# Kernel optimization log

Hardware: AMD Instinct MI355X
Metric: run time of the kernel (lower is better)

Reference implementation:

```python
import jax, jax.numpy as jnp
import numpy as np

N = 10000
E = 320000
D = 256
EPS = 1e-5

def layer_norm(x, g, b):
    mu = jnp.mean(x, axis=-1, keepdims=True)
    var = jnp.mean(jnp.square(x - mu), axis=-1, keepdims=True)
    return (x - mu) * jax.lax.rsqrt(var + EPS) * g + b

def linear(x, w, b):
    # w: [in, out]
    return x @ w + b

def setup_inputs() -> dict:
    key = jax.random.key(0)
    ks = jax.random.split(key, 20)
    s = 1.0 / np.sqrt(D)
    inp = {
        'x': jax.random.normal(ks[0], (N, D), jnp.float32),
        'edge_index': jax.random.randint(ks[1], (2, E), 0, N, jnp.int64),
        'edge_weight': jax.random.normal(ks[2], (E,), jnp.float32),
        'wq': jax.random.normal(ks[3], (D, D), jnp.float32) * s,
        'bq': jnp.zeros((D,), jnp.float32),
        'wk': jax.random.normal(ks[4], (D, D), jnp.float32) * s,
        'bk': jnp.zeros((D,), jnp.float32),
        'wv': jax.random.normal(ks[5], (D, D), jnp.float32) * s,
        'bv': jnp.zeros((D,), jnp.float32),
        'ws': jax.random.normal(ks[6], (D, D), jnp.float32) * s,
        'bs': jnp.zeros((D,), jnp.float32),
        'we': jax.random.normal(ks[7], (1, 1), jnp.float32),
        'be': jnp.zeros((1,), jnp.float32),
        'g1': jnp.ones((D,), jnp.float32),
        'b1': jnp.zeros((D,), jnp.float32),
        'g2': jnp.ones((D,), jnp.float32),
        'b2': jnp.zeros((D,), jnp.float32),
        'w_ff1': jax.random.normal(ks[8], (D, 2 * D), jnp.float32) * s,
        'b_ff1': jnp.zeros((2 * D,), jnp.float32),
        'w_ff2': jax.random.normal(ks[9], (2 * D, D), jnp.float32) * (1.0 / np.sqrt(2 * D)),
        'b_ff2': jnp.zeros((D,), jnp.float32),
    }
    return inp

def reference(x, edge_index, edge_weight, wq, bq, wk, bk, wv, bv, ws, bs, we, be,
              g1, b1, g2, b2, w_ff1, b_ff1, w_ff2, b_ff2):
    n = x.shape[0]
    scale = x.shape[-1] ** (-0.5)
    q = linear(x, wq, bq)
    k = linear(x, wk, bk)
    v = linear(x, wv, bv)
    src, dst = edge_index[0], edge_index[1]
    # per-edge attention scores: dot(q[dst], k[src]) * scale
    scores = jnp.sum(q[dst] * k[src], axis=-1) * scale
    scores = scores + (edge_weight[:, None] @ we + be)[:, 0]
    # two-pass segment softmax over dst
    seg_max = jax.ops.segment_max(scores, dst, num_segments=n)
    exp_s = jnp.exp(scores - seg_max[dst])
    denom = jax.ops.segment_sum(exp_s, dst, num_segments=n)
    attn = exp_s / jnp.maximum(denom[dst], 1e-12)
    # scatter-add weighted messages
    message = v[src] * attn[:, None]  # [E, D]
    out = jax.ops.segment_sum(message, dst, num_segments=n)
    x = layer_norm(x + out + linear(x, ws, bs), g1, b1)
    ffn = linear(jax.nn.gelu(linear(x, w_ff1, b_ff1)), w_ff2, b_ff2)
    x = layer_norm(x + ffn, g2, b2)
    return x
```

## Files before the change

kernel.cpp:

```cpp
#include <hip/hip_runtime.h>
#include <math.h>

#define N_NODES 10000
#define N_EDGES 320000
#define DIM 256
#define BCAP 128

#define P_PARTS 250
#define NPP 40
#define PCAP 2048
#define EPT 16

typedef __attribute__((ext_vector_type(8))) short bf16x8;
typedef __attribute__((ext_vector_type(4))) float fx4;

typedef __attribute__((address_space(3))) unsigned lds_u32;
typedef __attribute__((address_space(1))) const unsigned gbl_u32;


__device__ __forceinline__ float gelu_tanh(float x) {
  const float k0 = 0.7978845608028654f;
  float x3 = x * x * x;
  return 0.5f * x * (1.0f + tanhf(k0 * (x + 0.044715f * x3)));
}

__device__ __forceinline__ unsigned short f2bf(float f) {
  unsigned u = __float_as_uint(f);
  unsigned r = 0x7FFFu + ((u >> 16) & 1u);
  return (unsigned short)((u + r) >> 16);
}

__device__ __forceinline__ float bf_lo(unsigned u) { return __uint_as_float(u << 16); }
__device__ __forceinline__ float bf_hi(unsigned u) { return __uint_as_float(u & 0xFFFF0000u); }


#define SEG_QKVS 262144
#define SEG_FF1 131072
#define SEG_FF2 131072
#define SEG_BIAS 1024
#define SEG_CONV 320000
#define SEG_ZCNT 256
#define PREP_TOTAL (SEG_QKVS + SEG_FF1 + SEG_FF2 + SEG_BIAS + SEG_CONV + SEG_ZCNT)

__global__ __launch_bounds__(256) void prep_all_kernel(
    const float* __restrict__ wq, const float* __restrict__ wk,
    const float* __restrict__ wv, const float* __restrict__ ws,
    const float* __restrict__ bq, const float* __restrict__ bk,
    const float* __restrict__ bv, const float* __restrict__ bs,
    const float* __restrict__ wff1, const float* __restrict__ wff2,
    const float* __restrict__ x,
    unsigned short* __restrict__ wt_qkvs, float* __restrict__ bias_qkvs,
    unsigned short* __restrict__ wt_ff1, unsigned short* __restrict__ wt_ff2,
    unsigned short* __restrict__ xb, unsigned* __restrict__ pcnt) {
  int id = blockIdx.x * 256 + threadIdx.x;
  if (id < SEG_QKVS) {
    const int n = id >> 8, k = id & 255;
    const float* w = (n < 256) ? wq : (n < 512) ? wk : (n < 768) ? wv : ws;
    wt_qkvs[id] = f2bf(w[k * 256 + (n & 255)]);
    return;
  }
  id -= SEG_QKVS;
  if (id < SEG_FF1) {
    const int n = id >> 8, k = id & 255;
    wt_ff1[id] = f2bf(wff1[k * 512 + n]);
    return;
  }
  id -= SEG_FF1;
  if (id < SEG_FF2) {
    const int n = id >> 9, k = id & 511;
    wt_ff2[id] = f2bf(wff2[k * 256 + n]);
    return;
  }
  id -= SEG_FF2;
  if (id < SEG_BIAS) {
    bias_qkvs[id] = (id < 256) ? bq[id] : (id < 512) ? bk[id & 255]
                    : (id < 768) ? bv[id & 255] : bs[id & 255];
    return;
  }
  id -= SEG_BIAS;
  if (id < SEG_CONV) {
    const int base = id * 8;
    float4 a = *(const float4*)(x + base);
    float4 b = *(const float4*)(x + base + 4);
    unsigned short h[8] = {f2bf(a.x), f2bf(a.y), f2bf(a.z), f2bf(a.w),
                           f2bf(b.x), f2bf(b.y), f2bf(b.z), f2bf(b.w)};
    *(uint4*)(xb + base) = *(const uint4*)h;
    return;
  }
  id -= SEG_CONV;
  if (id < SEG_ZCNT) pcnt[id] = 0u;
}

__global__ __launch_bounds__(512) void scatter_p1(
    const int* __restrict__ ei, const float* __restrict__ ew,
    const float* __restrict__ we, const float* __restrict__ be,
    unsigned* __restrict__ pcnt, uint2* __restrict__ pbuf) {
  __shared__ unsigned lcnt[P_PARTS];
  __shared__ unsigned lbase[P_PARTS];
  const int tid = threadIdx.x;
  for (int i = tid; i < P_PARTS; i += 512) lcnt[i] = 0;
  __syncthreads();
  const float wes = we[0], bes = be[0];
  const int e0 = blockIdx.x * (512 * EPT);

  unsigned pp[EPT];
  unsigned rr[EPT];
  unsigned sv[EPT];
  float ebv[EPT];
#pragma unroll
  for (int j = 0; j < EPT; j++) {
    const int e = e0 + j * 512 + tid;
    pp[j] = 0;
    rr[j] = 0xFFFFFFFFu;
    if (e < N_EDGES) {
      const int dst = ei[N_EDGES + e];
      const int src = ei[e];
      const int p = dst / NPP;
      sv[j] = (unsigned)dst | ((unsigned)src << 16);
      ebv[j] = fmaf(ew[e], wes, bes);
      pp[j] = (unsigned)p;
      rr[j] = atomicAdd(&lcnt[p], 1u);
    }
  }
  __syncthreads();
  for (int i = tid; i < P_PARTS; i += 512) {
    const unsigned c = lcnt[i];
    lbase[i] = c ? atomicAdd(&pcnt[i], c) : 0u;
  }
  __syncthreads();
#pragma unroll
  for (int j = 0; j < EPT; j++) {
    if (rr[j] != 0xFFFFFFFFu) {
      const unsigned pos = lbase[pp[j]] + rr[j];
      if (pos < PCAP) {
        uint2 rec;
        rec.x = sv[j];
        rec.y = __float_as_uint(ebv[j]);
        pbuf[(size_t)pp[j] * PCAP + pos] = rec;
      }
    }
  }
}

__global__ __launch_bounds__(256) void scatter_p2(
    const unsigned* __restrict__ pcnt, const uint2* __restrict__ pbuf,
    unsigned* __restrict__ cnt, uint2* __restrict__ es_csr) {
  __shared__ unsigned lcnt[NPP];
  const int p = blockIdx.x;
  const int tid = threadIdx.x;
  if (tid < NPP) lcnt[tid] = 0;
  __syncthreads();
  const int n0 = p * NPP;
  const int tot = min((int)pcnt[p], PCAP);
  for (int i = tid; i < tot; i += 256) {
    const uint2 rec = pbuf[(size_t)p * PCAP + i];
    const int dst = (int)(rec.x & 0xFFFFu);
    const int src = (int)(rec.x >> 16);
    const unsigned r = atomicAdd(&lcnt[dst - n0], 1u);
    if (r < BCAP) {
      uint2 o;
      o.x = (unsigned)src;
      o.y = rec.y;
      es_csr[(size_t)dst * BCAP + r] = o;
    }
  }
  __syncthreads();
  if (tid < NPP) cnt[n0 + tid] = lcnt[tid];
}

template <int GELU, int WF32, int WB16, int SPLIT>
__global__ __launch_bounds__(256) void mfma_gemm(
    const unsigned short* __restrict__ A, int lda,
    const unsigned short* __restrict__ Bt,
    const float* __restrict__ bias,
    const float* __restrict__ xres,
    float* __restrict__ C, int ldc,
    unsigned short* __restrict__ Cb, int ldcb,
    int M, int K) {
  __shared__ char lds[32768];
  const int tid = threadIdx.x;

  const int l = tid & 63;
  const int wid = tid >> 6;
  const int wrow = (wid & 1) * 32;
  const int wcol = (wid >> 1) * 32;
  const int bm = blockIdx.y * 64;
  const int bn = blockIdx.x * 64;

  fx4 acc[2][2];
#pragma unroll
  for (int i = 0; i < 2; i++)
#pragma unroll
    for (int j = 0; j < 2; j++) acc[i][j] = (fx4)(0.0f);

#define STAGE(BUFOFF, KB)                                                      \
  {                                                                            \
    _Pragma("unroll") for (int i = 0; i < 2; i++) {                            \
      const int id = i * 256 + tid;                                            \
      const int row = id >> 3;                                                 \
      const int ccs = (id & 7) ^ (row & 7);                                    \
      __builtin_amdgcn_global_load_lds(                                        \
          (gbl_u32*)(A + (size_t)(bm + row) * lda + (KB) + ccs * 8),           \
          (lds_u32*)(lds + (BUFOFF) + id * 16), 16, 0, 0);                     \
    }                                                                          \
    _Pragma("unroll") for (int i = 0; i < 2; i++) {                            \
      const int id = i * 256 + tid;                                            \
      const int row = id >> 3;                                                 \
      const int ccs = (id & 7) ^ (row & 7);                                    \
      __builtin_amdgcn_global_load_lds(                                        \
          (gbl_u32*)(Bt + (size_t)(bn + row) * K + (KB) + ccs * 8),            \
          (lds_u32*)(lds + (BUFOFF) + 8192 + id * 16), 16, 0, 0);              \
    }                                                                          \
  }

  STAGE(0, 0);

  unsigned cur = 0;
  for (int kb = 0; kb < K; kb += 64) {
    if (kb + 64 < K) {
      STAGE((cur ^ 1) * 16384, kb + 64);
      asm volatile("s_waitcnt vmcnt(4)" ::: "memory");
    } else {
      asm volatile("s_waitcnt vmcnt(0)" ::: "memory");
    }
    __builtin_amdgcn_s_barrier();
    __builtin_amdgcn_sched_barrier(0);

    const char* As = lds + cur * 16384;
    const char* Bs = As + 8192;
#pragma unroll
    for (int kk = 0; kk < 2; kk++) {
      const int kbyte = (kk * 64 + ((l >> 4) << 4)) ^ ((l & 7) << 4);
      bf16x8 af[2], bg[2];
#pragma unroll
      for (int f = 0; f < 2; f++) {
        const int ar = wrow + f * 16 + (l & 15);
        af[f] = *(const bf16x8*)(As + ar * 128 + kbyte);
        const int br = wcol + f * 16 + (l & 15);
        bg[f] = *(const bf16x8*)(Bs + br * 128 + kbyte);
      }
#pragma unroll
      for (int fr = 0; fr < 2; fr++)
#pragma unroll
        for (int fc = 0; fc < 2; fc++)
          acc[fr][fc] = __builtin_amdgcn_mfma_f32_16x16x32_bf16(
              bg[fc], af[fr], acc[fr][fc], 0, 0, 0);
    }
    __builtin_amdgcn_s_barrier();
    cur ^= 1;
  }
#undef STAGE

#pragma unroll
  for (int fr = 0; fr < 2; fr++) {
    const int m = bm + wrow + fr * 16 + (l & 15);
    if (m < M) {
#pragma unroll
      for (int fc = 0; fc < 2; fc++) {
        const int n0 = bn + wcol + fc * 16 + ((l >> 4) << 2);
        const float4 b4 = *(const float4*)(bias + n0);
        fx4 v = acc[fr][fc];
        float o0 = v[0] + b4.x;
        float o1 = v[1] + b4.y;
        float o2 = v[2] + b4.z;
        float o3 = v[3] + b4.w;
        if (GELU) {
          o0 = gelu_tanh(o0); o1 = gelu_tanh(o1);
          o2 = gelu_tanh(o2); o3 = gelu_tanh(o3);
        }
        if (SPLIT) {
          const int seg = n0 >> 8, nn = n0 & 255;
          if (seg == 3) {
            const float4 xr = *(const float4*)(xres + (size_t)m * 256 + nn);
            float4 w;
            w.x = o0 + xr.x; w.y = o1 + xr.y; w.z = o2 + xr.z; w.w = o3 + xr.w;
            *(float4*)(C + (size_t)m * 256 + nn) = w;
          } else {
            uint2 pk;
            pk.x = (unsigned)f2bf(o0) | ((unsigned)f2bf(o1) << 16);
            pk.y = (unsigned)f2bf(o2) | ((unsigned)f2bf(o3) << 16);
            *(uint2*)(Cb + (size_t)seg * (N_NODES * DIM) + (size_t)m * 256 + nn) = pk;
          }
        } else {
          if (WF32) {
            float4 w; w.x = o0; w.y = o1; w.z = o2; w.w = o3;
            *(float4*)(C + (size_t)m * ldc + n0) = w;
          }
          if (WB16) {
            uint2 pk;
            pk.x = (unsigned)f2bf(o0) | ((unsigned)f2bf(o1) << 16);
            pk.y = (unsigned)f2bf(o2) | ((unsigned)f2bf(o3) << 16);
            *(uint2*)(Cb + (size_t)m * ldcb + n0) = pk;
          }
        }
      }
    }
  }
}

__global__ __launch_bounds__(64) void agg_fused_kernel(
    const unsigned* __restrict__ cnt, const uint2* __restrict__ es_csr,
    const unsigned short* __restrict__ qb,
    const unsigned short* __restrict__ kb, const unsigned short* __restrict__ vb,
    const float* __restrict__ sbuf,
    const float* __restrict__ g, const float* __restrict__ b,
    float* __restrict__ out, unsigned short* __restrict__ outb) {
  const int node = blockIdx.x;
  const int lane = threadIdx.x;
  const int grp = lane >> 4;
  const int t = lane & 15;
  const int start = node * BCAP;
  const int deg = min((int)cnt[node], BCAP);
  const int end = start + deg;

  const uint4 qA = *(const uint4*)(qb + (size_t)node * 256 + t * 16);
  const uint4 qB = *(const uint4*)(qb + (size_t)node * 256 + t * 16 + 8);
  float qf[16];
  qf[0] = bf_lo(qA.x);  qf[1] = bf_hi(qA.x);
  qf[2] = bf_lo(qA.y);  qf[3] = bf_hi(qA.y);
  qf[4] = bf_lo(qA.z);  qf[5] = bf_hi(qA.z);
  qf[6] = bf_lo(qA.w);  qf[7] = bf_hi(qA.w);
  qf[8] = bf_lo(qB.x);  qf[9] = bf_hi(qB.x);
  qf[10] = bf_lo(qB.y); qf[11] = bf_hi(qB.y);
  qf[12] = bf_lo(qB.z); qf[13] = bf_hi(qB.z);
  qf[14] = bf_lo(qB.w); qf[15] = bf_hi(qB.w);

  float m = -3.4e38f, dsum = 0.f;
  float a0 = 0.f, a1 = 0.f, a2 = 0.f, a3 = 0.f;

  int ea = start + grp * 2;
  int eb_ = ea + 1;
  bool va = ea < end, vbd = eb_ < end;
  int sa = 0, sb = 0;
  float ba = 0.f, bb = 0.f;
  if (va) { const uint2 es = es_csr[ea]; sa = (int)es.x; ba = __uint_as_float(es.y); }
  if (vbd) { const uint2 es = es_csr[eb_]; sb = (int)es.x; bb = __uint_as_float(es.y); }
  uint4 kAa = *(const uint4*)(kb + (size_t)sa * 256 + t * 16);
  uint4 kBa = *(const uint4*)(kb + (size_t)sa * 256 + t * 16 + 8);
  uint4 kAb = *(const uint4*)(kb + (size_t)sb * 256 + t * 16);
  uint4 kBb = *(const uint4*)(kb + (size_t)sb * 256 + t * 16 + 8);

  for (int base = start; base < end; base += 8) {
    const int s0 = __shfl(sa, 0), s1 = __shfl(sa, 16);
    const int s2 = __shfl(sa, 32), s3 = __shfl(sa, 48);
    const int s4 = __shfl(sb, 0), s5 = __shfl(sb, 16);
    const int s6 = __shfl(sb, 32), s7 = __shfl(sb, 48);
    const uint2 v0 = *(const uint2*)(vb + (size_t)s0 * 256 + lane * 4);
    const uint2 v1 = *(const uint2*)(vb + (size_t)s1 * 256 + lane * 4);
    const uint2 v2 = *(const uint2*)(vb + (size_t)s2 * 256 + lane * 4);
    const uint2 v3 = *(const uint2*)(vb + (size_t)s3 * 256 + lane * 4);
    const uint2 v4 = *(const uint2*)(vb + (size_t)s4 * 256 + lane * 4);
    const uint2 v5 = *(const uint2*)(vb + (size_t)s5 * 256 + lane * 4);
    const uint2 v6 = *(const uint2*)(vb + (size_t)s6 * 256 + lane * 4);
    const uint2 v7 = *(const uint2*)(vb + (size_t)s7 * 256 + lane * 4);

    const int na = base + 8 + grp * 2;
    const int nb = na + 1;
    const bool va_n = na < end, vb_n = nb < end;
    int sa_n = 0, sb_n = 0;
    float ba_n = 0.f, bb_n = 0.f;
    if (va_n) { const uint2 es = es_csr[na]; sa_n = (int)es.x; ba_n = __uint_as_float(es.y); }
    if (vb_n) { const uint2 es = es_csr[nb]; sb_n = (int)es.x; bb_n = __uint_as_float(es.y); }

    float da = qf[0] * bf_lo(kAa.x);
    float db = qf[0] * bf_lo(kAb.x);
    da = fmaf(qf[1], bf_hi(kAa.x), da);  db = fmaf(qf[1], bf_hi(kAb.x), db);
    da = fmaf(qf[2], bf_lo(kAa.y), da);  db = fmaf(qf[2], bf_lo(kAb.y), db);
    da = fmaf(qf[3], bf_hi(kAa.y), da);  db = fmaf(qf[3], bf_hi(kAb.y), db);
    da = fmaf(qf[4], bf_lo(kAa.z), da);  db = fmaf(qf[4], bf_lo(kAb.z), db);
    da = fmaf(qf[5], bf_hi(kAa.z), da);  db = fmaf(qf[5], bf_hi(kAb.z), db);
    da = fmaf(qf[6], bf_lo(kAa.w), da);  db = fmaf(qf[6], bf_lo(kAb.w), db);
    da = fmaf(qf[7], bf_hi(kAa.w), da);  db = fmaf(qf[7], bf_hi(kAb.w), db);
    da = fmaf(qf[8], bf_lo(kBa.x), da);  db = fmaf(qf[8], bf_lo(kBb.x), db);
    da = fmaf(qf[9], bf_hi(kBa.x), da);  db = fmaf(qf[9], bf_hi(kBb.x), db);
    da = fmaf(qf[10], bf_lo(kBa.y), da); db = fmaf(qf[10], bf_lo(kBb.y), db);
    da = fmaf(qf[11], bf_hi(kBa.y), da); db = fmaf(qf[11], bf_hi(kBb.y), db);
    da = fmaf(qf[12], bf_lo(kBa.z), da); db = fmaf(qf[12], bf_lo(kBb.z), db);
    da = fmaf(qf[13], bf_hi(kBa.z), da); db = fmaf(qf[13], bf_hi(kBb.z), db);
    da = fmaf(qf[14], bf_lo(kBa.w), da); db = fmaf(qf[14], bf_lo(kBb.w), db);
    da = fmaf(qf[15], bf_hi(kBa.w), da); db = fmaf(qf[15], bf_hi(kBb.w), db);
    da += __shfl_xor(da, 1);  db += __shfl_xor(db, 1);
    da += __shfl_xor(da, 2);  db += __shfl_xor(db, 2);
    da += __shfl_xor(da, 4);  db += __shfl_xor(db, 4);
    da += __shfl_xor(da, 8);  db += __shfl_xor(db, 8);
    const float sca = va ? fmaf(da, 0.0625f, ba) : -3.4e38f;
    const float scb = vbd ? fmaf(db, 0.0625f, bb) : -3.4e38f;

    const uint4 kAa_n = *(const uint4*)(kb + (size_t)sa_n * 256 + t * 16);
    const uint4 kBa_n = *(const uint4*)(kb + (size_t)sa_n * 256 + t * 16 + 8);
    const uint4 kAb_n = *(const uint4*)(kb + (size_t)sb_n * 256 + t * 16);
    const uint4 kBb_n = *(const uint4*)(kb + (size_t)sb_n * 256 + t * 16 + 8);

    const float c0 = __shfl(sca, 0), c1 = __shfl(sca, 16);
    const float c2 = __shfl(sca, 32), c3 = __shfl(sca, 48);
    const float c4 = __shfl(scb, 0), c5 = __shfl(scb, 16);
    const float c6 = __shfl(scb, 32), c7 = __shfl(scb, 48);

    const float mx = fmaxf(fmaxf(fmaxf(c0, c1), fmaxf(c2, c3)),
                           fmaxf(fmaxf(c4, c5), fmaxf(c6, c7)));
    const float mn = fmaxf(m, mx);
    const float scale = __expf(m - mn);
    const float w0 = __expf(c0 - mn), w1 = __expf(c1 - mn);
    const float w2 = __expf(c2 - mn), w3 = __expf(c3 - mn);
    const float w4 = __expf(c4 - mn), w5 = __expf(c5 - mn);
    const float w6 = __expf(c6 - mn), w7 = __expf(c7 - mn);
    dsum = fmaf(dsum, scale, ((w0 + w1) + (w2 + w3)) + ((w4 + w5) + (w6 + w7)));

    float t0 = a0 * scale;
    t0 = fmaf(w0, bf_lo(v0.x), t0); t0 = fmaf(w1, bf_lo(v1.x), t0);
    t0 = fmaf(w2, bf_lo(v2.x), t0); t0 = fmaf(w3, bf_lo(v3.x), t0);
    t0 = fmaf(w4, bf_lo(v4.x), t0); t0 = fmaf(w5, bf_lo(v5.x), t0);
    t0 = fmaf(w6, bf_lo(v6.x), t0); t0 = fmaf(w7, bf_lo(v7.x), t0);
    a0 = t0;
    float t1 = a1 * scale;
    t1 = fmaf(w0, bf_hi(v0.x), t1); t1 = fmaf(w1, bf_hi(v1.x), t1);
    t1 = fmaf(w2, bf_hi(v2.x), t1); t1 = fmaf(w3, bf_hi(v3.x), t1);
    t1 = fmaf(w4, bf_hi(v4.x), t1); t1 = fmaf(w5, bf_hi(v5.x), t1);
    t1 = fmaf(w6, bf_hi(v6.x), t1); t1 = fmaf(w7, bf_hi(v7.x), t1);
    a1 = t1;
    float t2 = a2 * scale;
    t2 = fmaf(w0, bf_lo(v0.y), t2); t2 = fmaf(w1, bf_lo(v1.y), t2);
    t2 = fmaf(w2, bf_lo(v2.y), t2); t2 = fmaf(w3, bf_lo(v3.y), t2);
    t2 = fmaf(w4, bf_lo(v4.y), t2); t2 = fmaf(w5, bf_lo(v5.y), t2);
    t2 = fmaf(w6, bf_lo(v6.y), t2); t2 = fmaf(w7, bf_lo(v7.y), t2);
    a2 = t2;
    float t3 = a3 * scale;
    t3 = fmaf(w0, bf_hi(v0.y), t3); t3 = fmaf(w1, bf_hi(v1.y), t3);
    t3 = fmaf(w2, bf_hi(v2.y), t3); t3 = fmaf(w3, bf_hi(v3.y), t3);
    t3 = fmaf(w4, bf_hi(v4.y), t3); t3 = fmaf(w5, bf_hi(v5.y), t3);
    t3 = fmaf(w6, bf_hi(v6.y), t3); t3 = fmaf(w7, bf_hi(v7.y), t3);
    a3 = t3;
    m = mn;

    sa = sa_n; sb = sb_n;
    ba = ba_n; bb = bb_n;
    va = va_n; vbd = vb_n;
    kAa = kAa_n; kBa = kBa_n;
    kAb = kAb_n; kBb = kBb_n;
  }
  const float inv = 1.0f / fmaxf(dsum, 1e-12f);

  const float4 sv = *(const float4*)(sbuf + (size_t)node * 256 + lane * 4);
  float r0 = a0 * inv + sv.x;
  float r1 = a1 * inv + sv.y;
  float r2 = a2 * inv + sv.z;
  float r3 = a3 * inv + sv.w;

  float sum = r0 + r1 + r2 + r3;
#pragma unroll
  for (int off = 32; off > 0; off >>= 1) sum += __shfl_xor(sum, off);
  const float mu = sum * (1.0f / 256.0f);
  const float d0 = r0 - mu, d1 = r1 - mu, d2 = r2 - mu, d3 = r3 - mu;
  float vs = d0 * d0 + d1 * d1 + d2 * d2 + d3 * d3;
#pragma unroll
  for (int off = 32; off > 0; off >>= 1) vs += __shfl_xor(vs, off);
  const float rs = rsqrtf(vs * (1.0f / 256.0f) + 1e-5f);

  const float4 gv = *(const float4*)(g + lane * 4);
  const float4 bv = *(const float4*)(b + lane * 4);
  float4 o;
  o.x = d0 * rs * gv.x + bv.x;
  o.y = d1 * rs * gv.y + bv.y;
  o.z = d2 * rs * gv.z + bv.z;
  o.w = d3 * rs * gv.w + bv.w;
  *(float4*)(out + (size_t)node * 256 + lane * 4) = o;
  uint2 pk;
  pk.x = (unsigned)f2bf(o.x) | ((unsigned)f2bf(o.y) << 16);
  pk.y = (unsigned)f2bf(o.z) | ((unsigned)f2bf(o.w) << 16);
  *(uint2*)(outb + (size_t)node * 256 + lane * 4) = pk;
}


__global__ __launch_bounds__(256) void ln2_kernel(
    const float* __restrict__ x1, const float* __restrict__ y,
    const float* __restrict__ g, const float* __restrict__ b,
    float* __restrict__ out) {
  __shared__ float red[4];
  const int row = blockIdx.x;
  const int t = threadIdx.x;
  float v = x1[(size_t)row * 256 + t] + y[(size_t)row * 256 + t];
  float s = v;
#pragma unroll
  for (int off = 32; off > 0; off >>= 1) s += __shfl_xor(s, off);
  if ((t & 63) == 0) red[t >> 6] = s;
  __syncthreads();
  float tot = red[0] + red[1] + red[2] + red[3];
  __syncthreads();
  const float mu = tot * (1.0f / 256.0f);
  const float d = v - mu;
  float vs = d * d;
#pragma unroll
  for (int off = 32; off > 0; off >>= 1) vs += __shfl_xor(vs, off);
  if ((t & 63) == 0) red[t >> 6] = vs;
  __syncthreads();
  float vtot = red[0] + red[1] + red[2] + red[3];
  const float r = rsqrtf(vtot * (1.0f / 256.0f) + 1e-5f);
  out[(size_t)row * 256 + t] = d * r * g[t] + b[t];
}


extern "C" void kernel_launch(void* const* d_in, const int* in_sizes, int n_in,
                              void* d_out, int out_size, void* d_ws,
                              size_t ws_size, hipStream_t stream) {
  const float* x = (const float*)d_in[0];
  const int* ei = (const int*)d_in[1];
  const float* ew = (const float*)d_in[2];
  const float* wq = (const float*)d_in[3];
  const float* bq = (const float*)d_in[4];
  const float* wk = (const float*)d_in[5];
  const float* bk = (const float*)d_in[6];
  const float* wv = (const float*)d_in[7];
  const float* bv = (const float*)d_in[8];
  const float* wsm = (const float*)d_in[9];
  const float* bs = (const float*)d_in[10];
  const float* we = (const float*)d_in[11];
  const float* be = (const float*)d_in[12];
  const float* g1 = (const float*)d_in[13];
  const float* b1 = (const float*)d_in[14];
  const float* g2 = (const float*)d_in[15];
  const float* b2 = (const float*)d_in[16];
  const float* wff1 = (const float*)d_in[17];
  const float* bff1 = (const float*)d_in[18];
  const float* wff2 = (const float*)d_in[19];
  const float* bff2 = (const float*)d_in[20];
  float* out = (float*)d_out;

  unsigned short* qb = (unsigned short*)d_ws;
  unsigned short* kbp = qb + 2560000;
  unsigned short* vbp = qb + 5120000;
  float* sbuf = (float*)(qb + 7680000);
  uint2* es_csr = (uint2*)(sbuf + 2560000);
  unsigned* cnt = (unsigned*)(es_csr + (size_t)N_NODES * BCAP);
  float* x1 = (float*)(cnt + N_NODES);
  float* y = x1 + 2560000;
  unsigned short* x1b = (unsigned short*)(y + 2560000);
  unsigned short* h_b = x1b + 2560000;
  unsigned short* xb = h_b;
  unsigned short* wt_qkvs = h_b + 5120000;
  unsigned short* wt_ff1 = wt_qkvs + 262144;
  unsigned short* wt_ff2 = wt_ff1 + 131072;
  float* bias_qkvs = (float*)(wt_ff2 + 131072);
  unsigned* pcnt = (unsigned*)(bias_qkvs + 1024);
  uint2* pbuf = (uint2*)(pcnt + 256);

  dim3 blk(256);
  const int mb = (N_NODES + 63) / 64;

  prep_all_kernel<<<(PREP_TOTAL + 255) / 256, blk, 0, stream>>>(
      wq, wk, wv, wsm, bq, bk, bv, bs, wff1, wff2, x,
      wt_qkvs, bias_qkvs, wt_ff1, wt_ff2, xb, pcnt);

  scatter_p1<<<(N_EDGES + 512 * EPT - 1) / (512 * EPT), dim3(512), 0, stream>>>(
      ei, ew, we, be, pcnt, pbuf);
  scatter_p2<<<P_PARTS, blk, 0, stream>>>(pcnt, pbuf, cnt, es_csr);

  mfma_gemm<0, 0, 0, 1><<<dim3(16, mb), blk, 0, stream>>>(
      xb, 256, wt_qkvs, bias_qkvs, x, sbuf, 0, qb, 0, N_NODES, 256);

  agg_fused_kernel<<<N_NODES, dim3(64), 0, stream>>>(
      cnt, es_csr, qb, kbp, vbp, sbuf, g1, b1, x1, x1b);

  mfma_gemm<1, 0, 1, 0><<<dim3(8, mb), blk, 0, stream>>>(
      x1b, 256, wt_ff1, bff1, nullptr, (float*)nullptr, 0, h_b, 512, N_NODES, 256);

  mfma_gemm<0, 1, 0, 0><<<dim3(4, mb), blk, 0, stream>>>(
      h_b, 512, wt_ff2, bff2, nullptr, y, 256, (unsigned short*)nullptr, 0, N_NODES, 512);

  ln2_kernel<<<N_NODES, blk, 0, stream>>>(x1, y, g2, b2, out);
}
```

Measured before the change: 125.6 us.

## Replace double-buffered LDS GEMM with register-resident A and full-K B tile in LDS

Rewrites the MFMA GEMM so each wave keeps its 16-row A slice for the whole K range in registers, loaded straight from global memory. The block's whole B (weight) tile is staged into swizzled LDS once, with a single barrier. This removes the per-K-step staging loop and its barriers. In exchange it uses more registers, larger LDS (up to 32KB), smaller per-wave M tiles, and no overlap between loads and compute. FF2 now uses 32-column tiles, doubling the grid width.

```diff
diff --git a/kernel.cpp b/kernel.cpp
--- a/kernel.cpp
+++ b/kernel.cpp
@@ -13,9 +13,6 @@
 
 typedef __attribute__((ext_vector_type(8))) short bf16x8;
 typedef __attribute__((ext_vector_type(4))) float fx4;
-
-typedef __attribute__((address_space(3))) unsigned lds_u32;
-typedef __attribute__((address_space(1))) const unsigned gbl_u32;
 
 
 __device__ __forceinline__ float gelu_tanh(float x) {
@@ -168,131 +165,100 @@
   if (tid < NPP) cnt[n0 + tid] = lcnt[tid];
 }
 
-template <int GELU, int WF32, int WB16, int SPLIT>
-__global__ __launch_bounds__(256) void mfma_gemm(
-    const unsigned short* __restrict__ A, int lda,
+template <int K, int NT, int GELU, int WF32, int WB16, int SPLIT>
+__global__ __launch_bounds__(256) void stream_gemm(
+    const unsigned short* __restrict__ A,
     const unsigned short* __restrict__ Bt,
     const float* __restrict__ bias,
     const float* __restrict__ xres,
     float* __restrict__ C, int ldc,
     unsigned short* __restrict__ Cb, int ldcb,
-    int M, int K) {
-  __shared__ char lds[32768];
+    int M) {
+  __shared__ char lds[NT * K * 2];
   const int tid = threadIdx.x;
-
   const int l = tid & 63;
-  const int wid = tid >> 6;
-  const int wrow = (wid & 1) * 32;
-  const int wcol = (wid >> 1) * 32;
+  const int w = tid >> 6;
+  const int bn = blockIdx.x * NT;
   const int bm = blockIdx.y * 64;
-  const int bn = blockIdx.x * 64;
-
-  fx4 acc[2][2];
-#pragma unroll
-  for (int i = 0; i < 2; i++)
-#pragma unroll
-    for (int j = 0; j < 2; j++) acc[i][j] = (fx4)(0.0f);
-
-#define STAGE(BUFOFF, KB)                                                      \
-  {                                                                            \
-    _Pragma("unroll") for (int i = 0; i < 2; i++) {                            \
-      const int id = i * 256 + tid;                                            \
-      const int row = id >> 3;                                                 \
-      const int ccs = (id & 7) ^ (row & 7);                                    \
-      __builtin_amdgcn_global_load_lds(                                        \
-          (gbl_u32*)(A + (size_t)(bm + row) * lda + (KB) + ccs * 8),           \
-          (lds_u32*)(lds + (BUFOFF) + id * 16), 16, 0, 0);                     \
-    }                                                                          \
-    _Pragma("unroll") for (int i = 0; i < 2; i++) {                            \
-      const int id = i * 256 + tid;                                            \
-      const int row = id >> 3;                                                 \
-      const int ccs = (id & 7) ^ (row & 7);                                    \
-      __builtin_amdgcn_global_load_lds(                                        \
-          (gbl_u32*)(Bt + (size_t)(bn + row) * K + (KB) + ccs * 8),            \
-          (lds_u32*)(lds + (BUFOFF) + 8192 + id * 16), 16, 0, 0);              \
-    }                                                                          \
-  }
-
-  STAGE(0, 0);
-
-  unsigned cur = 0;
-  for (int kb = 0; kb < K; kb += 64) {
-    if (kb + 64 < K) {
-      STAGE((cur ^ 1) * 16384, kb + 64);
-      asm volatile("s_waitcnt vmcnt(4)" ::: "memory");
+  const int wr = bm + w * 16;
+
+  constexpr int KS = K / 32;
+  constexpr int NF = NT / 16;
+  constexpr int CPR = K / 8;
+  constexpr int CPT = (NT * CPR) / 256;
+
+  uint4 af[KS];
+  {
+    const unsigned short* arow = A + (size_t)(wr + (l & 15)) * K + ((l >> 4) * 8);
+#pragma unroll
+    for (int kk = 0; kk < KS; kk++)
+      af[kk] = *(const uint4*)(arow + kk * 32);
+  }
+
+#pragma unroll
+  for (int i = 0; i < CPT; i++) {
+    const int ch = i * 256 + tid;
+    const int n = ch / CPR;
+    const int c = ch % CPR;
+    const uint4 v = *(const uint4*)(Bt + (size_t)(bn + n) * K + c * 8);
+    *(uint4*)(lds + n * (K * 2) + ((c * 16) ^ ((n & 7) << 4))) = v;
+  }
+  __syncthreads();
+
+  fx4 acc[NF];
+#pragma unroll
+  for (int nf = 0; nf < NF; nf++) acc[nf] = (fx4)(0.0f);
+#pragma unroll
+  for (int kk = 0; kk < KS; kk++) {
+    const bf16x8 a = *(const bf16x8*)(&af[kk]);
+#pragma unroll
+    for (int nf = 0; nf < NF; nf++) {
+      const int n = nf * 16 + (l & 15);
+      const bf16x8 b = *(const bf16x8*)(
+          lds + n * (K * 2) + ((kk * 64 + ((l >> 4) << 4)) ^ ((n & 7) << 4)));
+      acc[nf] = __builtin_amdgcn_mfma_f32_16x16x32_bf16(b, a, acc[nf], 0, 0, 0);
+    }
+  }
+
+  const int m = wr + (l & 15);
+  if (m >= M) return;
+  const int seg = bn >> 8;
+#pragma unroll
+  for (int nf = 0; nf < NF; nf++) {
+    const int n0 = bn + nf * 16 + ((l >> 4) << 2);
+    const float4 b4 = *(const float4*)(bias + n0);
+    fx4 v = acc[nf];
+    float o0 = v[0] + b4.x;
+    float o1 = v[1] + b4.y;
+    float o2 = v[2] + b4.z;
+    float o3 = v[3] + b4.w;
+    if (GELU) {
+      o0 = gelu_tanh(o0); o1 = gelu_tanh(o1);
+      o2 = gelu_tanh(o2); o3 = gelu_tanh(o3);
+    }
+    if (SPLIT) {
+      const int nn = n0 & 255;
+      if (seg == 3) {
+        const float4 xr = *(const float4*)(xres + (size_t)m * 256 + nn);
+        float4 wv;
+        wv.x = o0 + xr.x; wv.y = o1 + xr.y; wv.z = o2 + xr.z; wv.w = o3 + xr.w;
+        *(float4*)(C + (size_t)m * 256 + nn) = wv;
+      } else {
+        uint2 pk;
+        pk.x = (unsigned)f2bf(o0) | ((unsigned)f2bf(o1) << 16);
+        pk.y = (unsigned)f2bf(o2) | ((unsigned)f2bf(o3) << 16);
+        *(uint2*)(Cb + (size_t)seg * (N_NODES * DIM) + (size_t)m * 256 + nn) = pk;
+      }
     } else {
-      asm volatile("s_waitcnt vmcnt(0)" ::: "memory");
-    }
-    __builtin_amdgcn_s_barrier();
-    __builtin_amdgcn_sched_barrier(0);
-
-    const char* As = lds + cur * 16384;
-    const char* Bs = As + 8192;
-#pragma unroll
-    for (int kk = 0; kk < 2; kk++) {
-      const int kbyte = (kk * 64 + ((l >> 4) << 4)) ^ ((l & 7) << 4);
-      bf16x8 af[2], bg[2];
-#pragma unroll
-      for (int f = 0; f < 2; f++) {
-        const int ar = wrow + f * 16 + (l & 15);
-        af[f] = *(const bf16x8*)(As + ar * 128 + kbyte);
-        const int br = wcol + f * 16 + (l & 15);
-        bg[f] = *(const bf16x8*)(Bs + br * 128 + kbyte);
+      if (WF32) {
+        float4 wv; wv.x = o0; wv.y = o1; wv.z = o2; wv.w = o3;
+        *(float4*)(C + (size_t)m * ldc + n0) = wv;
       }
-#pragma unroll
-      for (int fr = 0; fr < 2; fr++)
-#pragma unroll
-        for (int fc = 0; fc < 2; fc++)
-          acc[fr][fc] = __builtin_amdgcn_mfma_f32_16x16x32_bf16(
-              bg[fc], af[fr], acc[fr][fc], 0, 0, 0);
-    }
-    __builtin_amdgcn_s_barrier();
-    cur ^= 1;
-  }
-#undef STAGE
-
-#pragma unroll
-  for (int fr = 0; fr < 2; fr++) {
-    const int m = bm + wrow + fr * 16 + (l & 15);
-    if (m < M) {
-#pragma unroll
-      for (int fc = 0; fc < 2; fc++) {
-        const int n0 = bn + wcol + fc * 16 + ((l >> 4) << 2);
-        const float4 b4 = *(const float4*)(bias + n0);
-        fx4 v = acc[fr][fc];
-        float o0 = v[0] + b4.x;
-        float o1 = v[1] + b4.y;
-        float o2 = v[2] + b4.z;
-        float o3 = v[3] + b4.w;
-        if (GELU) {
-          o0 = gelu_tanh(o0); o1 = gelu_tanh(o1);
-          o2 = gelu_tanh(o2); o3 = gelu_tanh(o3);
-        }
-        if (SPLIT) {
-          const int seg = n0 >> 8, nn = n0 & 255;
-          if (seg == 3) {
-            const float4 xr = *(const float4*)(xres + (size_t)m * 256 + nn);
-            float4 w;
-            w.x = o0 + xr.x; w.y = o1 + xr.y; w.z = o2 + xr.z; w.w = o3 + xr.w;
-            *(float4*)(C + (size_t)m * 256 + nn) = w;
-          } else {
-            uint2 pk;
-            pk.x = (unsigned)f2bf(o0) | ((unsigned)f2bf(o1) << 16);
-            pk.y = (unsigned)f2bf(o2) | ((unsigned)f2bf(o3) << 16);
-            *(uint2*)(Cb + (size_t)seg * (N_NODES * DIM) + (size_t)m * 256 + nn) = pk;
-          }
-        } else {
-          if (WF32) {
-            float4 w; w.x = o0; w.y = o1; w.z = o2; w.w = o3;
-            *(float4*)(C + (size_t)m * ldc + n0) = w;
-          }
-          if (WB16) {
-            uint2 pk;
-            pk.x = (unsigned)f2bf(o0) | ((unsigned)f2bf(o1) << 16);
-            pk.y = (unsigned)f2bf(o2) | ((unsigned)f2bf(o3) << 16);
-            *(uint2*)(Cb + (size_t)m * ldcb + n0) = pk;
-          }
-        }
+      if (WB16) {
+        uint2 pk;
+        pk.x = (unsigned)f2bf(o0) | ((unsigned)f2bf(o1) << 16);
+        pk.y = (unsigned)f2bf(o2) | ((unsigned)f2bf(o3) << 16);
+        *(uint2*)(Cb + (size_t)m * ldcb + n0) = pk;
       }
     }
   }
@@ -478,7 +444,8 @@
   __shared__ float red[4];
   const int row = blockIdx.x;
   const int t = threadIdx.x;
-  float v = x1[(size_t)row * 256 + t] + y[(size_t)row * 256 + t];
+  const size_t idx = (size_t)row * 256 + t;
+  float v = x1[idx] + y[idx];
   float s = v;
 #pragma unroll
   for (int off = 32; off > 0; off >>= 1) s += __shfl_xor(s, off);
@@ -495,7 +462,7 @@
   __syncthreads();
   float vtot = red[0] + red[1] + red[2] + red[3];
   const float r = rsqrtf(vtot * (1.0f / 256.0f) + 1e-5f);
-  out[(size_t)row * 256 + t] = d * r * g[t] + b[t];
+  out[idx] = d * r * g[t] + b[t];
 }
 
 
@@ -554,17 +521,17 @@
       ei, ew, we, be, pcnt, pbuf);
   scatter_p2<<<P_PARTS, blk, 0, stream>>>(pcnt, pbuf, cnt, es_csr);
 
-  mfma_gemm<0, 0, 0, 1><<<dim3(16, mb), blk, 0, stream>>>(
-      xb, 256, wt_qkvs, bias_qkvs, x, sbuf, 0, qb, 0, N_NODES, 256);
+  stream_gemm<256, 64, 0, 0, 0, 1><<<dim3(16, mb), blk, 0, stream>>>(
+      xb, wt_qkvs, bias_qkvs, x, sbuf, 0, qb, 0, N_NODES);
 
   agg_fused_kernel<<<N_NODES, dim3(64), 0, stream>>>(
       cnt, es_csr, qb, kbp, vbp, sbuf, g1, b1, x1, x1b);
 
-  mfma_gemm<1, 0, 1, 0><<<dim3(8, mb), blk, 0, stream>>>(
-      x1b, 256, wt_ff1, bff1, nullptr, (float*)nullptr, 0, h_b, 512, N_NODES, 256);
-
-  mfma_gemm<0, 1, 0, 0><<<dim3(4, mb), blk, 0, stream>>>(
-      h_b, 512, wt_ff2, bff2, nullptr, y, 256, (unsigned short*)nullptr, 0, N_NODES, 512);
+  stream_gemm<256, 64, 1, 0, 1, 0><<<dim3(8, mb), blk, 0, stream>>>(
+      x1b, wt_ff1, bff1, nullptr, (float*)nullptr, 0, h_b, 512, N_NODES);
+
+  stream_gemm<512, 32, 0, 1, 0, 0><<<dim3(8, mb), blk, 0, stream>>>(
+      h_b, wt_ff2, bff2, nullptr, y, 256, (unsigned short*)nullptr, 0, N_NODES);
 
   ln2_kernel<<<N_NODES, blk, 0, stream>>>(x1, y, g2, b2, out);
 }
```

Result: slower. 140.5 us (+11.9%).

## Fuse both FFN GEMMs into one kernel keeping hidden activations in LDS

Applied to the files above, without the earlier changes.

Replaces the two FFN GEMM launches with a single kernel. Each 256-thread block computes a 16-row tile of the GELU hidden layer with MFMA, stores it as bf16 in swizzled shared memory, and then immediately runs the second GEMM from LDS. This removes the global write and reread of the 10000x512 hidden tensor and one launch. In exchange, weights are read directly from global memory with no LDS staging, and small 16-row tiles mean weight traffic is repeated across 625 blocks. Also includes a minor index cleanup in the final layer-norm kernel.

```diff
diff --git a/kernel.cpp b/kernel.cpp
--- a/kernel.cpp
+++ b/kernel.cpp
@@ -298,6 +298,83 @@
   }
 }
 
+__global__ __launch_bounds__(256) void ffn_fused(
+    const unsigned short* __restrict__ x1b,
+    const unsigned short* __restrict__ w1,
+    const float* __restrict__ b1,
+    const unsigned short* __restrict__ w2,
+    const float* __restrict__ b2,
+    float* __restrict__ y, int M) {
+  __shared__ char hlds[16 * 1024];
+  const int tid = threadIdx.x;
+  const int l = tid & 63;
+  const int wv = tid >> 6;
+  const int bm = blockIdx.x * 16;
+  const int ml = l & 15;
+  const int kc = l >> 4;
+  const int swz = (ml & 7) << 4;
+
+  uint4 af[8];
+  {
+    const unsigned short* ar = x1b + (size_t)(bm + ml) * 256 + kc * 8;
+#pragma unroll
+    for (int kk = 0; kk < 8; kk++) af[kk] = *(const uint4*)(ar + kk * 32);
+  }
+
+#pragma unroll
+  for (int cf = 0; cf < 8; cf++) {
+    const int nb = wv * 128 + cf * 16;
+    const unsigned short* br = w1 + (size_t)(nb + ml) * 256 + kc * 8;
+    fx4 acc = (fx4)(0.0f);
+#pragma unroll
+    for (int kk = 0; kk < 8; kk++) {
+      const uint4 bv = *(const uint4*)(br + kk * 32);
+      acc = __builtin_amdgcn_mfma_f32_16x16x32_bf16(
+          *(const bf16x8*)(&bv), *(const bf16x8*)(&af[kk]), acc, 0, 0, 0);
+    }
+    const int n0 = nb + kc * 4;
+    const float4 b4 = *(const float4*)(b1 + n0);
+    const float o0 = gelu_tanh(acc[0] + b4.x);
+    const float o1 = gelu_tanh(acc[1] + b4.y);
+    const float o2 = gelu_tanh(acc[2] + b4.z);
+    const float o3 = gelu_tanh(acc[3] + b4.w);
+    uint2 pk;
+    pk.x = (unsigned)f2bf(o0) | ((unsigned)f2bf(o1) << 16);
+    pk.y = (unsigned)f2bf(o2) | ((unsigned)f2bf(o3) << 16);
+    *(uint2*)(hlds + ml * 1024 + ((n0 * 2) ^ swz)) = pk;
+  }
+  __syncthreads();
+
+  fx4 acc2[4];
+#pragma unroll
+  for (int cf = 0; cf < 4; cf++) acc2[cf] = (fx4)(0.0f);
+#pragma unroll
+  for (int kk = 0; kk < 16; kk++) {
+    const bf16x8 a = *(const bf16x8*)(
+        hlds + ml * 1024 + (((kc * 16) + kk * 64) ^ swz));
+#pragma unroll
+    for (int cf = 0; cf < 4; cf++) {
+      const int n = wv * 64 + cf * 16 + ml;
+      const uint4 bv = *(const uint4*)(w2 + (size_t)n * 512 + kc * 8 + kk * 32);
+      acc2[cf] = __builtin_amdgcn_mfma_f32_16x16x32_bf16(
+          *(const bf16x8*)(&bv), a, acc2[cf], 0, 0, 0);
+    }
+  }
+  const int m = bm + ml;
+  if (m >= M) return;
+#pragma unroll
+  for (int cf = 0; cf < 4; cf++) {
+    const int n0 = wv * 64 + cf * 16 + kc * 4;
+    const float4 b4 = *(const float4*)(b2 + n0);
+    float4 o;
+    o.x = acc2[cf][0] + b4.x;
+    o.y = acc2[cf][1] + b4.y;
+    o.z = acc2[cf][2] + b4.z;
+    o.w = acc2[cf][3] + b4.w;
+    *(float4*)(y + (size_t)m * 256 + n0) = o;
+  }
+}
+
 __global__ __launch_bounds__(64) void agg_fused_kernel(
     const unsigned* __restrict__ cnt, const uint2* __restrict__ es_csr,
     const unsigned short* __restrict__ qb,
@@ -478,7 +555,8 @@
   __shared__ float red[4];
   const int row = blockIdx.x;
   const int t = threadIdx.x;
-  float v = x1[(size_t)row * 256 + t] + y[(size_t)row * 256 + t];
+  const size_t idx = (size_t)row * 256 + t;
+  float v = x1[idx] + y[idx];
   float s = v;
 #pragma unroll
   for (int off = 32; off > 0; off >>= 1) s += __shfl_xor(s, off);
@@ -495,7 +573,7 @@
   __syncthreads();
   float vtot = red[0] + red[1] + red[2] + red[3];
   const float r = rsqrtf(vtot * (1.0f / 256.0f) + 1e-5f);
-  out[(size_t)row * 256 + t] = d * r * g[t] + b[t];
+  out[idx] = d * r * g[t] + b[t];
 }
 
 
@@ -560,11 +638,8 @@
   agg_fused_kernel<<<N_NODES, dim3(64), 0, stream>>>(
       cnt, es_csr, qb, kbp, vbp, sbuf, g1, b1, x1, x1b);
 
-  mfma_gemm<1, 0, 1, 0><<<dim3(8, mb), blk, 0, stream>>>(
-      x1b, 256, wt_ff1, bff1, nullptr, (float*)nullptr, 0, h_b, 512, N_NODES, 256);
-
-  mfma_gemm<0, 1, 0, 0><<<dim3(4, mb), blk, 0, stream>>>(
-      h_b, 512, wt_ff2, bff2, nullptr, y, 256, (unsigned short*)nullptr, 0, N_NODES, 512);
+  ffn_fused<<<dim3((N_NODES + 15) / 16), blk, 0, stream>>>(
+      x1b, wt_ff1, bff1, wt_ff2, bff2, y, N_NODES);
 
   ln2_kernel<<<N_NODES, blk, 0, stream>>>(x1, y, g2, b2, out);
 }
```

Result: slower. 145.7 us (+16.0%).

## Fold CSR bucket scatter into QKVS GEMM launch and shrink edges per thread

Applied to the files above, without the earlier changes.

Removes the standalone scatter_p2 kernel and runs its per-partition bucket fill as the first 250 blocks of the QKVS GEMM, whose remaining blocks are remapped onto a flattened 1D grid. The two independent jobs now share one launch and can overlap on the GPU, saving a kernel launch and its tail. EPT also drops from 16 to 4, giving scatter_p1 four times as many blocks with less work each. This trades better parallelism for more global atomics on the partition counters.

```diff
diff --git a/kernel.cpp b/kernel.cpp
--- a/kernel.cpp
+++ b/kernel.cpp
@@ -9,7 +9,7 @@
 #define P_PARTS 250
 #define NPP 40
 #define PCAP 2048
-#define EPT 16
+#define EPT 4
 
 typedef __attribute__((ext_vector_type(8))) short bf16x8;
 typedef __attribute__((ext_vector_type(4))) float fx4;
@@ -142,32 +142,6 @@
   }
 }
 
-__global__ __launch_bounds__(256) void scatter_p2(
-    const unsigned* __restrict__ pcnt, const uint2* __restrict__ pbuf,
-    unsigned* __restrict__ cnt, uint2* __restrict__ es_csr) {
-  __shared__ unsigned lcnt[NPP];
-  const int p = blockIdx.x;
-  const int tid = threadIdx.x;
-  if (tid < NPP) lcnt[tid] = 0;
-  __syncthreads();
-  const int n0 = p * NPP;
-  const int tot = min((int)pcnt[p], PCAP);
-  for (int i = tid; i < tot; i += 256) {
-    const uint2 rec = pbuf[(size_t)p * PCAP + i];
-    const int dst = (int)(rec.x & 0xFFFFu);
-    const int src = (int)(rec.x >> 16);
-    const unsigned r = atomicAdd(&lcnt[dst - n0], 1u);
-    if (r < BCAP) {
-      uint2 o;
-      o.x = (unsigned)src;
-      o.y = rec.y;
-      es_csr[(size_t)dst * BCAP + r] = o;
-    }
-  }
-  __syncthreads();
-  if (tid < NPP) cnt[n0 + tid] = lcnt[tid];
-}
-
 template <int GELU, int WF32, int WB16, int SPLIT>
 __global__ __launch_bounds__(256) void mfma_gemm(
     const unsigned short* __restrict__ A, int lda,
@@ -176,16 +150,51 @@
     const float* __restrict__ xres,
     float* __restrict__ C, int ldc,
     unsigned short* __restrict__ Cb, int ldcb,
-    int M, int K) {
+    int M, int K,
+    const unsigned* __restrict__ pcnt, const uint2* __restrict__ pbuf,
+    unsigned* __restrict__ cnt, uint2* __restrict__ es_csr) {
   __shared__ char lds[32768];
   const int tid = threadIdx.x;
+
+  if (SPLIT) {
+    const int bid = blockIdx.x;
+    if (bid < P_PARTS) {
+      unsigned* lcnt = (unsigned*)lds;
+      if (tid < NPP) lcnt[tid] = 0;
+      __syncthreads();
+      const int n0 = bid * NPP;
+      const int tot = min((int)pcnt[bid], PCAP);
+      for (int i = tid; i < tot; i += 256) {
+        const uint2 rec = pbuf[(size_t)bid * PCAP + i];
+        const int dst = (int)(rec.x & 0xFFFFu);
+        const int src = (int)(rec.x >> 16);
+        const unsigned r = atomicAdd(&lcnt[dst - n0], 1u);
+        if (r < BCAP) {
+          uint2 o;
+          o.x = (unsigned)src;
+          o.y = rec.y;
+          es_csr[(size_t)dst * BCAP + r] = o;
+        }
+      }
+      __syncthreads();
+      if (tid < NPP) cnt[n0 + tid] = lcnt[tid];
+      return;
+    }
+  }
 
   const int l = tid & 63;
   const int wid = tid >> 6;
   const int wrow = (wid & 1) * 32;
   const int wcol = (wid >> 1) * 32;
-  const int bm = blockIdx.y * 64;
-  const int bn = blockIdx.x * 64;
+  int bm, bn;
+  if (SPLIT) {
+    const int bid2 = blockIdx.x - P_PARTS;
+    bm = (bid2 >> 4) * 64;
+    bn = (bid2 & 15) * 64;
+  } else {
+    bm = blockIdx.y * 64;
+    bn = blockIdx.x * 64;
+  }
 
   fx4 acc[2][2];
 #pragma unroll
@@ -552,19 +561,21 @@
 
   scatter_p1<<<(N_EDGES + 512 * EPT - 1) / (512 * EPT), dim3(512), 0, stream>>>(
       ei, ew, we, be, pcnt, pbuf);
-  scatter_p2<<<P_PARTS, blk, 0, stream>>>(pcnt, pbuf, cnt, es_csr);
-
-  mfma_gemm<0, 0, 0, 1><<<dim3(16, mb), blk, 0, stream>>>(
-      xb, 256, wt_qkvs, bias_qkvs, x, sbuf, 0, qb, 0, N_NODES, 256);
+
+  mfma_gemm<0, 0, 0, 1><<<dim3(P_PARTS + 16 * mb), blk, 0, stream>>>(
+      xb, 256, wt_qkvs, bias_qkvs, x, sbuf, 0, qb, 0, N_NODES, 256,
+      pcnt, pbuf, cnt, es_csr);
 
   agg_fused_kernel<<<N_NODES, dim3(64), 0, stream>>>(
       cnt, es_csr, qb, kbp, vbp, sbuf, g1, b1, x1, x1b);
 
   mfma_gemm<1, 0, 1, 0><<<dim3(8, mb), blk, 0, stream>>>(
-      x1b, 256, wt_ff1, bff1, nullptr, (float*)nullptr, 0, h_b, 512, N_NODES, 256);
+      x1b, 256, wt_ff1, bff1, nullptr, (float*)nullptr, 0, h_b, 512, N_NODES, 256,
+      nullptr, nullptr, nullptr, nullptr);
 
   mfma_gemm<0, 1, 0, 0><<<dim3(4, mb), blk, 0, stream>>>(
-      h_b, 512, wt_ff2, bff2, nullptr, y, 256, (unsigned short*)nullptr, 0, N_NODES, 512);
+      h_b, 512, wt_ff2, bff2, nullptr, y, 256, (unsigned short*)nullptr, 0, N_NODES, 512,
+      nullptr, nullptr, nullptr, nullptr);
 
   ln2_kernel<<<N_NODES, blk, 0, stream>>>(x1, y, g2, b2, out);
 }
```

Measured after the change: 117.8 us (median of 2 runs). -6.2%, faster.
